# Performance work log

Measured on AMD Instinct MI355X. Metric: run time of the kernel, lower is better.

Reference implementation:

```python
import jax, jax.numpy as jnp
import numpy as np

NUM_ITER = 5  # num_iterations
M, N, B = 972, 1944, 8  # check_matrix_row, check_matrix_column, unit_batch_size
ROW_DEG = 8  # check-node degree of the sparse parity matrix


def setup_inputs() -> dict:
    key = jax.random.key(0)
    # sparse binary parity-check matrix H (constant Tanner graph)
    rng = np.random.default_rng(0)
    H = np.zeros((M, N), np.float32)
    for i in range(M):
        H[i, rng.choice(N, ROW_DEG, replace=False)] = 1.0
    soft_input = 2.0 * jax.random.normal(key, (B, N), dtype=jnp.float32)  # channel LLRs
    check_weight = jnp.array([-1.07], dtype=jnp.float32)  # NMS init constant
    return {"soft_input": soft_input, "H": jnp.asarray(H), "check_weight": check_weight}


def _bp_iteration(cv, soft_input, H, check_weight):
    # ---- compute_vc (NMS: bit weight == 1.0) ----
    total = jnp.sum(cv, axis=1) + soft_input              # [B, N]
    vc = total[:, None, :] * H - cv                       # [B, M, N]
    # ---- compute_cv (min-sum branch) ----
    back = jnp.where(H == 0, -1e30 - 1.0, 0.0)[None]      # mask non-edges
    a = jnp.clip(jnp.abs(vc), 0.0, 1e30)
    dec = -a + back
    top2, _ = jax.lax.top_k(dec, 2)                       # [B, M, 2]
    min1 = (-top2[..., 0])[:, :, None] * H                # row min broadcast on edges
    min2 = (-top2[..., 1])[:, :, None] * H                # row second-min
    result = jnp.where(a > min1, min1, min2)              # exclude-self min
    sign_info = (1.0 - H)[None] + vc
    s = jnp.sign(sign_info)
    tot_sign = jnp.prod(s, axis=2)[:, :, None] * H
    result_sign = tot_sign * s                            # exclude-self sign product
    w = jax.nn.softplus(check_weight)                     # scalar NMS factor
    cv_new = result * jax.lax.stop_gradient(result_sign) * w
    return cv_new


def reference(soft_input, H, check_weight):
    Bn, n = soft_input.shape
    m = H.shape[0]
    cv0 = jnp.zeros((Bn, m, n), dtype=soft_input.dtype)

    def body(cv, _):
        return _bp_iteration(cv, soft_input, H, check_weight), None

    cv, _ = jax.lax.scan(body, cv0, None, length=NUM_ITER)
    # marginalize
    soft_output = jnp.sum(cv, axis=1) + soft_input
    return soft_output
```

## Files before the change

### kernel.cpp

```cpp
#include <hip/hip_runtime.h>
#include <math.h>

#define MM 972
#define NN 1944
#define BB 8
#define RD 8
#define NITER 5
#define MAXD 16
#define POISON 0xAAAAAAAAu

__device__ __forceinline__ void emit_edge(int m, int n, int* cnt,
                                          unsigned* __restrict__ col_cnt,
                                          int* __restrict__ row_edges) {
    int j = atomicAdd(cnt, 1);
    unsigned k = atomicAdd(&col_cnt[n], 1u) - POISON;
    if (k > MAXD - 1u) k = MAXD - 1u;
    int kk = (int)k;
    int phys = (((((kk >> 2) + n + (n >> 1)) & 3) << 2) | (kk & 3));
    row_edges[m * RD + j] = n * MAXD + phys;
}

__global__ __launch_bounds__(256) void build_adj(const float* __restrict__ H,
                                                 unsigned* __restrict__ col_cnt,
                                                 int* __restrict__ row_edges) {
    const int m = blockIdx.x;
    __shared__ int cnt;
    if (threadIdx.x == 0) cnt = 0;
    __syncthreads();
    const float4* H4 = (const float4*)(H + (size_t)m * NN);
    for (int q = threadIdx.x; q < NN / 4; q += blockDim.x) {
        float4 h = H4[q];
        int n = 4 * q;
        if (h.x != 0.0f) emit_edge(m, n + 0, &cnt, col_cnt, row_edges);
        if (h.y != 0.0f) emit_edge(m, n + 1, &cnt, col_cnt, row_edges);
        if (h.z != 0.0f) emit_edge(m, n + 2, &cnt, col_cnt, row_edges);
        if (h.w != 0.0f) emit_edge(m, n + 3, &cnt, col_cnt, row_edges);
    }
}

__global__ __launch_bounds__(1024, 1) void decode(const float* __restrict__ soft,
                                                  const float* __restrict__ cwp,
                                                  const unsigned* __restrict__ col_cnt,
                                                  const int* __restrict__ row_edges,
                                                  float* __restrict__ out) {
    __shared__ __align__(16) float cvc[NN * MAXD];
    __shared__ float tot[NN];

    const int b = blockIdx.x;
    const int t = threadIdx.x;
    const float* soft_b = soft + b * NN;

    int rc[RD], rs[RD];
    float cv[RD];
    if (t < MM) {
        const int* rep = row_edges + t * RD;
#pragma unroll
        for (int j = 0; j < RD; ++j) {
            int s = rep[j];
            rs[j] = s;
            rc[j] = s >> 4;
            cv[j] = 0.0f;
        }
    }

    const int n0 = t;
    const int n1 = t + 1024;
    const bool has1 = (n1 < NN);
    const int n1c = has1 ? n1 : 0;
    const float s0 = soft_b[n0];
    const float s1 = has1 ? soft_b[n1] : 0.0f;
    const int g0 = (n0 + (n0 >> 1)) & 3;
    const int g1 = (n1c + (n1c >> 1)) & 3;
    const unsigned d0 = col_cnt[n0] - POISON;
    const unsigned d1 = has1 ? (col_cnt[n1] - POISON) : 0u;
    const int C0 = ((int)min(d0, (unsigned)MAXD) + 3) >> 2;
    const int C1 = ((int)min(d1, (unsigned)MAXD) + 3) >> 2;

    const float w = log1pf(expf(cwp[0]));

    float4* cv4 = (float4*)cvc;
#pragma unroll
    for (int i = 0; i < 8; ++i) {
        int idx = t + i * 1024;
        if (idx < NN * MAXD / 4) cv4[idx] = make_float4(0.f, 0.f, 0.f, 0.f);
    }
    tot[n0] = s0;
    if (has1) tot[n1] = s1;
    __syncthreads();

#pragma unroll
    for (int it = 0; it < NITER; ++it) {
        if (t < MM) {
            unsigned ab[RD];
            unsigned sg[RD];
            unsigned m1 = 0x7f800000u, m2 = 0x7f800000u, sx = 0u;
#pragma unroll
            for (int j = 0; j < RD; ++j) {
                float vv = tot[rc[j]] - cv[j];
                unsigned u = __float_as_uint(vv);
                sg[j] = u;
                sx ^= u;
                unsigned a = u & 0x7fffffffu;
                ab[j] = a;
                if (a < m1) { m2 = m1; m1 = a; }
                else if (a < m2) { m2 = a; }
            }
            const float we = (m1 == 0u) ? 0.0f : w;
            const unsigned sxb = sx & 0x80000000u;
#pragma unroll
            for (int j = 0; j < RD; ++j) {
                unsigned mag = (ab[j] > m1) ? m1 : m2;
                unsigned sb  = (sg[j] ^ sxb) & 0x80000000u;
                float nc = __uint_as_float(mag | sb) * we;
                cv[j] = nc;
                cvc[rs[j]] = nc;
            }
        }
        __syncthreads();

        float a0 = 0.0f, a1 = 0.0f;
#pragma unroll
        for (int i = 0; i < 4; ++i) {
            if (i < C0) {
                float4 q = cv4[n0 * 4 + ((i + g0) & 3)];
                a0 += (q.x + q.y) + (q.z + q.w);
            }
            if (i < C1) {
                float4 q = cv4[n1c * 4 + ((i + g1) & 3)];
                a1 += (q.x + q.y) + (q.z + q.w);
            }
        }
        const float t0 = s0 + a0;
        const float t1 = s1 + a1;
        if (it == NITER - 1) {
            out[b * NN + n0] = t0;
            if (has1) out[b * NN + n1] = t1;
        } else {
            tot[n0] = t0;
            if (has1) tot[n1] = t1;
            __syncthreads();
        }
    }
}

extern "C" void kernel_launch(void* const* d_in, const int* in_sizes, int n_in,
                              void* d_out, int out_size, void* d_ws, size_t ws_size,
                              hipStream_t stream) {
    const float* soft = (const float*)d_in[0];
    const float* H    = (const float*)d_in[1];
    const float* cw   = (const float*)d_in[2];
    float* out = (float*)d_out;

    unsigned* col_cnt = (unsigned*)d_ws;
    int* row_edges    = (int*)(col_cnt + NN);

    build_adj<<<MM, 256, 0, stream>>>(H, col_cnt, row_edges);
    decode<<<BB, 1024, 0, stream>>>(soft, cw, col_cnt, row_edges, out);
}
```

Baseline: 75.00 us.

## Sort variable nodes by column degree to reduce wavefront divergence in column sums

```diff
diff --git a/kernel.cpp b/kernel.cpp
--- a/kernel.cpp
+++ b/kernel.cpp
@@ -45,9 +45,14 @@
                                                   float* __restrict__ out) {
     __shared__ __align__(16) float cvc[NN * MAXD];
     __shared__ float tot[NN];
+    __shared__ int perm[NN];
+    __shared__ int bin_cnt[5];
+    __shared__ int bin_base[5];
 
     const int b = blockIdx.x;
     const int t = threadIdx.x;
+    const int lane = t & 63;
+    const unsigned long long lt_mask = (1ull << lane) - 1ull;
     const float* soft_b = soft + b * NN;
 
     int rc[RD], rs[RD];
@@ -63,53 +68,107 @@
         }
     }
 
-    const int n0 = t;
-    const int n1 = t + 1024;
-    const bool has1 = (n1 < NN);
-    const int n1c = has1 ? n1 : 0;
-    const float s0 = soft_b[n0];
-    const float s1 = has1 ? soft_b[n1] : 0.0f;
-    const int g0 = (n0 + (n0 >> 1)) & 3;
-    const int g1 = (n1c + (n1c >> 1)) & 3;
-    const unsigned d0 = col_cnt[n0] - POISON;
-    const unsigned d1 = has1 ? (col_cnt[n1] - POISON) : 0u;
-    const int C0 = ((int)min(d0, (unsigned)MAXD) + 3) >> 2;
-    const int C1 = ((int)min(d1, (unsigned)MAXD) + 3) >> 2;
+    const int p0 = t;
+    const int p1 = t + 1024;
+    const bool h1 = (p1 < NN);
+    const float sp0 = soft_b[p0];
+    const float sp1 = h1 ? soft_b[p1] : 0.0f;
+    const unsigned dr0 = col_cnt[p0] - POISON;
+    const unsigned dr1 = h1 ? (col_cnt[p1] - POISON) : 0u;
+    const int de0 = (int)min(dr0, (unsigned)MAXD);
+    const int de1 = (int)min(dr1, (unsigned)MAXD);
+    const int cl0 = (de0 + 3) >> 2;
+    const int cl1 = h1 ? ((de1 + 3) >> 2) : -1;
 
     const float w = log1pf(expf(cwp[0]));
 
+    if (t < 5) { bin_cnt[t] = 0; }
+    tot[p0] = sp0;
+    if (h1) tot[p1] = sp1;
+    if (de0 < (cl0 << 2)) {
+        const int g = (p0 + (p0 >> 1)) & 3;
+        const int base = p0 * MAXD + ((((cl0 - 1) + g) & 3) << 2);
+        for (int k = de0 & 3; k < 4; ++k) cvc[base + k] = 0.0f;
+    }
+    if (h1 && de1 < (cl1 << 2)) {
+        const int g = (p1 + (p1 >> 1)) & 3;
+        const int base = p1 * MAXD + ((((cl1 - 1) + g) & 3) << 2);
+        for (int k = de1 & 3; k < 4; ++k) cvc[base + k] = 0.0f;
+    }
+    __syncthreads();
+
+#pragma unroll
+    for (int c = 0; c < 5; ++c) {
+        unsigned long long m0 = __ballot(cl0 == c);
+        if ((cl0 == c) && lane == __ffsll((unsigned long long)m0) - 1)
+            atomicAdd(&bin_cnt[c], (int)__popcll(m0));
+        unsigned long long m1 = __ballot(cl1 == c);
+        if ((cl1 == c) && lane == __ffsll((unsigned long long)m1) - 1)
+            atomicAdd(&bin_cnt[c], (int)__popcll(m1));
+    }
+    __syncthreads();
+    if (t == 0) {
+        int s = 0;
+#pragma unroll
+        for (int c = 0; c < 5; ++c) { bin_base[c] = s; s += bin_cnt[c]; }
+    }
+    __syncthreads();
+#pragma unroll
+    for (int c = 0; c < 5; ++c) {
+        unsigned long long m0 = __ballot(cl0 == c);
+        if (cl0 == c) {
+            int leader = __ffsll((unsigned long long)m0) - 1;
+            int wb = 0;
+            if (lane == leader) wb = atomicAdd(&bin_base[c], (int)__popcll(m0));
+            wb = __shfl(wb, leader);
+            perm[wb + (int)__popcll(m0 & lt_mask)] = (p0 << 3) | c;
+        }
+        unsigned long long m1 = __ballot(cl1 == c);
+        if (cl1 == c) {
+            int leader = __ffsll((unsigned long long)m1) - 1;
+            int wb = 0;
+            if (lane == leader) wb = atomicAdd(&bin_base[c], (int)__popcll(m1));
+            wb = __shfl(wb, leader);
+            perm[wb + (int)__popcll(m1 & lt_mask)] = (p1 << 3) | c;
+        }
+    }
+    __syncthreads();
+
+    const int e0 = perm[p0];
+    const int e1 = h1 ? perm[p1] : 0;
+    const int nn0 = e0 >> 3;
+    const int C0 = e0 & 7;
+    const int nn1 = e1 >> 3;
+    const int C1 = h1 ? (e1 & 7) : 0;
+    const int g0 = (nn0 + (nn0 >> 1)) & 3;
+    const int g1 = (nn1 + (nn1 >> 1)) & 3;
+    const float s0 = tot[nn0];
+    const float s1 = h1 ? tot[nn1] : 0.0f;
     float4* cv4 = (float4*)cvc;
-#pragma unroll
-    for (int i = 0; i < 8; ++i) {
-        int idx = t + i * 1024;
-        if (idx < NN * MAXD / 4) cv4[idx] = make_float4(0.f, 0.f, 0.f, 0.f);
-    }
-    tot[n0] = s0;
-    if (has1) tot[n1] = s1;
-    __syncthreads();
-
-#pragma unroll
+
     for (int it = 0; it < NITER; ++it) {
         if (t < MM) {
-            unsigned ab[RD];
-            unsigned sg[RD];
-            unsigned m1 = 0x7f800000u, m2 = 0x7f800000u, sx = 0u;
+            float vv[RD];
+#pragma unroll
+            for (int j = 0; j < RD; ++j)
+                vv[j] = tot[rc[j]] - cv[j];
+            unsigned ab[RD], sg[RD];
+            unsigned m1v = 0x7f800000u, m2v = 0x7f800000u, sx = 0u;
 #pragma unroll
             for (int j = 0; j < RD; ++j) {
-                float vv = tot[rc[j]] - cv[j];
-                unsigned u = __float_as_uint(vv);
+                unsigned u = __float_as_uint(vv[j]);
                 sg[j] = u;
                 sx ^= u;
                 unsigned a = u & 0x7fffffffu;
                 ab[j] = a;
-                if (a < m1) { m2 = m1; m1 = a; }
-                else if (a < m2) { m2 = a; }
-            }
-            const float we = (m1 == 0u) ? 0.0f : w;
+                if (a < m1v) { m2v = m1v; m1v = a; }
+                else if (a < m2v) { m2v = a; }
+            }
+            const float we = (m1v == 0u) ? 0.0f : w;
             const unsigned sxb = sx & 0x80000000u;
 #pragma unroll
             for (int j = 0; j < RD; ++j) {
-                unsigned mag = (ab[j] > m1) ? m1 : m2;
+                unsigned mag = (ab[j] > m1v) ? m1v : m2v;
                 unsigned sb  = (sg[j] ^ sxb) & 0x80000000u;
                 float nc = __uint_as_float(mag | sb) * we;
                 cv[j] = nc;
@@ -122,25 +181,21 @@
 #pragma unroll
         for (int i = 0; i < 4; ++i) {
             if (i < C0) {
-                float4 q = cv4[n0 * 4 + ((i + g0) & 3)];
+                float4 q = cv4[nn0 * 4 + ((i + g0) & 3)];
                 a0 += (q.x + q.y) + (q.z + q.w);
             }
             if (i < C1) {
-                float4 q = cv4[n1c * 4 + ((i + g1) & 3)];
+                float4 q = cv4[nn1 * 4 + ((i + g1) & 3)];
                 a1 += (q.x + q.y) + (q.z + q.w);
             }
         }
-        const float t0 = s0 + a0;
-        const float t1 = s1 + a1;
-        if (it == NITER - 1) {
-            out[b * NN + n0] = t0;
-            if (has1) out[b * NN + n1] = t1;
-        } else {
-            tot[n0] = t0;
-            if (has1) tot[n1] = t1;
-            __syncthreads();
-        }
-    }
+        tot[nn0] = s0 + a0;
+        if (h1) tot[nn1] = s1 + a1;
+        __syncthreads();
+    }
+
+    out[b * NN + p0] = tot[p0];
+    if (h1) out[b * NN + p1] = tot[p1];
 }
 
 extern "C" void kernel_launch(void* const* d_in, const int* in_sizes, int n_in,
```

New measurement: 78.36 us. 4.5% more time.
